# Kernel tuning notes

Measured on AMD Instinct MI355X. Metric: run time of the kernel, lower is better.

The kernel has to match this reference:

```python
import jax, jax.numpy as jnp
import numpy as np

B, T, H = 64, 2048, 64  # basins, daily timesteps, MLP hidden width


def _mlp(x, W1, b1, W2, b2, W3, b3, W4, b4):
    # x: [..., 4] -> [..., 5]; tanh hidden layers, linear head
    h = jnp.tanh(x @ W1 + b1)
    h = jnp.tanh(h @ W2 + b2)
    h = jnp.tanh(h @ W3 + b3)
    return h @ W4 + b4


def _step(x):
    # smooth step function from the torch module
    return (jnp.tanh(5.0 * x) + 1.0) * 0.5


def _interp(series, t):
    # linear interpolation of per-basin forcing series [B, T] at scalar time t
    # (time grid is the integer daily grid 0..T-1, matching time_series)
    n = series.shape[1]
    i0 = jnp.clip(jnp.floor(t).astype(jnp.int32), 0, n - 2)
    frac = t - i0.astype(series.dtype)
    pair = jax.lax.dynamic_slice_in_dim(series, i0, 2, axis=1)  # [B, 2]
    return pair[:, 0] * (1.0 - frac) + pair[:, 1] * frac


def _forward(s_snow, s_water, precp_series, tmean_series, lday_series, time_series,
             W1, b1, W2, b2, W3, b3, W4, b4):
    params = (W1, b1, W2, b2, W3, b3, W4, b4)

    def rhs(t, y):  # y: [B, 2]
        s0, s1 = y[:, 0], y[:, 1]
        precp = _interp(precp_series, t)
        temp = _interp(tmean_series, t)
        lday = _interp(lday_series, t)
        o = _mlp(jnp.stack([s0, s1, precp, temp], axis=-1), *params)  # [B, 5]
        # scale_target_vars=True branch
        p_snow = jax.nn.relu(jnp.sinh(o[:, 0]) * _step(-temp))
        p_rain = jax.nn.relu(jnp.sinh(o[:, 1]))
        m = jax.nn.relu(_step(s0) * jnp.sinh(o[:, 2]))
        et = _step(s1) * jnp.exp(o[:, 3]) * lday
        q = _step(s1) * jnp.exp(o[:, 4])
        return jnp.stack([p_snow - m, p_rain + m - et - q], axis=-1)

    y0 = jnp.stack([s_snow[:, 0], s_water[:, 0]], axis=-1)  # [B, 2]
    t0s = time_series[:-1]
    dts = time_series[1:] - time_series[:-1]

    def scan_step(y, td):  # classic RK4 between consecutive grid points
        t0, dt = td
        half = dt * 0.5
        k1 = rhs(t0, y)
        k2 = rhs(t0 + half, y + half * k1)
        k3 = rhs(t0 + half, y + half * k2)
        k4 = rhs(t0 + dt, y + dt * k3)
        y_next = y + (dt / 6.0) * (k1 + 2.0 * k2 + 2.0 * k3 + k4)
        return y_next, y_next

    _, ys = jax.lax.scan(scan_step, y0, (t0s, dts))  # [T-1, B, 2]
    y_full = jnp.concatenate([y0[None], ys], axis=0)  # [T, B, 2]
    y_full = jnp.transpose(y_full, (1, 0, 2))  # [B, T, 2]

    # final NN pass over the integrated states + raw forcing series
    inputs_nn = jnp.stack(
        [y_full[..., 0], y_full[..., 1], precp_series, tmean_series], axis=-1)  # [B, T, 4]
    q_out = _mlp(inputs_nn, *params)[..., -1]  # [B, T] (last output column = q)
    return q_out


def setup_inputs() -> dict:
    key = jax.random.key(0)
    ks = jax.random.split(key, 9)
    return {
        "s_snow": jax.random.uniform(ks[0], (B, T), dtype=jnp.float32),
        "s_water": jax.random.uniform(ks[1], (B, T), dtype=jnp.float32),
        "precp_series": jax.random.uniform(ks[2], (B, T), dtype=jnp.float32),
        "tmean_series": jax.random.normal(ks[3], (B, T), dtype=jnp.float32),
        "lday_series": jax.random.uniform(ks[4], (B, T), dtype=jnp.float32) * 0.5,
        "time_series": jnp.arange(T, dtype=jnp.float32),
        "W1": jax.random.normal(ks[5], (4, H), dtype=jnp.float32) / jnp.sqrt(4.0),
        "b1": jnp.zeros((H,), jnp.float32),
        "W2": jax.random.normal(ks[6], (H, H), dtype=jnp.float32) / jnp.sqrt(float(H)),
        "b2": jnp.zeros((H,), jnp.float32),
        "W3": jax.random.normal(ks[7], (H, H), dtype=jnp.float32) / jnp.sqrt(float(H)),
        "b3": jnp.zeros((H,), jnp.float32),
        "W4": jax.random.normal(ks[8], (H, 5), dtype=jnp.float32) * (0.1 / jnp.sqrt(float(H))),
        "b4": jnp.zeros((5,), jnp.float32),
    }


def reference(s_snow, s_water, precp_series, tmean_series, lday_series, time_series,
              W1, b1, W2, b2, W3, b3, W4, b4):
    return _forward(s_snow, s_water, precp_series, tmean_series, lday_series,
                    time_series, W1, b1, W2, b2, W3, b3, W4, b4)
```

## Files before the change

kernel.cpp:

```cpp
#include <hip/hip_runtime.h>
#include <cmath>

#define LOG2E 1.44269504088896340736f
#define TMAX 2048

#if __has_builtin(__builtin_amdgcn_exp2f)
#define EXP2F(x) __builtin_amdgcn_exp2f(x)
#else
#define EXP2F(x) exp2f(x)
#endif
#if __has_builtin(__builtin_amdgcn_rcpf)
#define RCPF(x) __builtin_amdgcn_rcpf(x)
#else
#define RCPF(x) (1.0f / (x))
#endif

typedef float float2v __attribute__((ext_vector_type(2)));
typedef float float4v __attribute__((ext_vector_type(4)));

__device__ __forceinline__ float fexp(float x)  { return EXP2F(x * LOG2E); }
__device__ __forceinline__ float ftanh(float x) { return 1.0f - 2.0f * RCPF(1.0f + EXP2F(x * (2.0f * LOG2E))); }
__device__ __forceinline__ float fstep(float x) { return RCPF(1.0f + EXP2F(x * (-10.0f * LOG2E))); }
__device__ __forceinline__ float fsinh(float x) { float e = fexp(x); return 0.5f * (e - RCPF(e)); }

__device__ __forceinline__ int fadd_i(int a, int b) {
    return __builtin_bit_cast(int, __builtin_bit_cast(float, a) + __builtin_bit_cast(float, b));
}

__device__ __forceinline__ float wave_sum63(float x) {
    int v = __builtin_bit_cast(int, x);
    v = fadd_i(v, __builtin_amdgcn_update_dpp(0, v, 0x111, 0xF, 0xF, true));
    v = fadd_i(v, __builtin_amdgcn_update_dpp(0, v, 0x112, 0xF, 0xF, true));
    v = fadd_i(v, __builtin_amdgcn_update_dpp(0, v, 0x114, 0xF, 0xF, true));
    v = fadd_i(v, __builtin_amdgcn_update_dpp(0, v, 0x118, 0xF, 0xF, true));
    v = fadd_i(v, __builtin_amdgcn_update_dpp(0, v, 0x142, 0xA, 0xF, true));
    v = fadd_i(v, __builtin_amdgcn_update_dpp(0, v, 0x143, 0xC, 0xF, true));
    return __builtin_bit_cast(float, v);
}

__device__ __forceinline__ float rl(float x, int l) {
    return __builtin_bit_cast(float, __builtin_amdgcn_readlane(__builtin_bit_cast(int, x), l));
}

__device__ __forceinline__ float2v pk_fma(float2v a, float2v b, float2v c) {
    float2v d;
    asm("v_pk_fma_f32 %0, %1, %2, %3" : "=v"(d) : "v"(a), "v"(b), "v"(c));
    return d;
}

__device__ __forceinline__ float2v vlo(float4v v) { return __builtin_shufflevector(v, v, 0, 1); }
__device__ __forceinline__ float2v vhi(float4v v) { return __builtin_shufflevector(v, v, 2, 3); }

__global__ __launch_bounds__(256, 1)
void exphydro_kernel(const float* __restrict__ g_snow, const float* __restrict__ g_water,
                     const float* __restrict__ g_pr, const float* __restrict__ g_tm,
                     const float* __restrict__ g_ld, const float* __restrict__ g_t,
                     const float* __restrict__ W1, const float* __restrict__ b1,
                     const float* __restrict__ W2, const float* __restrict__ b2,
                     const float* __restrict__ W3, const float* __restrict__ b3,
                     const float* __restrict__ W4, const float* __restrict__ b4,
                     float* __restrict__ out, int T)
{
    const int tid  = threadIdx.x;
    const int lane = tid & 63;
    const int wid  = tid >> 6;
    const int b    = blockIdx.x;

    __shared__ __align__(16) float4v s_f[TMAX];
    __shared__ __align__(16) float hcopy[4][64];
    __shared__ __align__(16) float partA[4][64];
    __shared__ __align__(16) float partB[4][64];

    for (int i = tid; i < T; i += 256) {
        s_f[i] = float4v{g_pr[b * T + i], g_tm[b * T + i], g_ld[b * T + i], g_t[i]};
    }

    float w1r[4];
#pragma unroll
    for (int j = 0; j < 4; ++j) w1r[j] = W1[j * 64 + lane];
    float b1v = b1[lane];

    float2v w2s[8], w3s[8];
#pragma unroll
    for (int k = 0; k < 8; ++k) {
        int r = 16 * wid + 2 * k;
        w2s[k] = float2v{W2[r * 64 + lane], W2[(r + 1) * 64 + lane]};
        w3s[k] = float2v{W3[r * 64 + lane], W3[(r + 1) * 64 + lane]};
    }
    float b2v = (wid == 0) ? b2[lane] : 0.0f;
    float b3v = (wid == 0) ? b3[lane] : 0.0f;
    float w4r[5], b4r[5];
#pragma unroll
    for (int k = 0; k < 5; ++k) { w4r[k] = W4[lane * 5 + k]; b4r[k] = b4[k]; }

    __syncthreads();

    auto quarter_dot = [&](const float* hq, const float2v (&w)[8], float bias) -> float {
        float4v q0 = *reinterpret_cast<const float4v*>(hq + 0);
        float4v q1 = *reinterpret_cast<const float4v*>(hq + 4);
        float4v q2 = *reinterpret_cast<const float4v*>(hq + 8);
        float4v q3 = *reinterpret_cast<const float4v*>(hq + 12);
        float2v a0 = float2v{bias, 0.0f}, a1 = float2v{0.0f, 0.0f};
        a0 = pk_fma(w[0], vlo(q0), a0); a1 = pk_fma(w[1], vhi(q0), a1);
        a0 = pk_fma(w[2], vlo(q1), a0); a1 = pk_fma(w[3], vhi(q1), a1);
        a0 = pk_fma(w[4], vlo(q2), a0); a1 = pk_fma(w[5], vhi(q2), a1);
        a0 = pk_fma(w[6], vlo(q3), a0); a1 = pk_fma(w[7], vhi(q3), a1);
        float2v s = a0 + a1;
        return s.x + s.y;
    };

    auto mlp_o63 = [&](float h1, float* o) {
        float* hown = &hcopy[wid][0];
        const float* hq = hown + 16 * wid;
        hown[lane] = h1;
        partA[wid][lane] = quarter_dot(hq, w2s, b2v);
        __syncthreads();
        float h2 = ftanh((partA[0][lane] + partA[1][lane]) + (partA[2][lane] + partA[3][lane]));
        hown[lane] = h2;
        partB[wid][lane] = quarter_dot(hq, w3s, b3v);
        __syncthreads();
        float h3 = ftanh((partB[0][lane] + partB[1][lane]) + (partB[2][lane] + partB[3][lane]));
#pragma unroll
        for (int k = 0; k < 5; ++k) o[k] = wave_sum63(w4r[k] * h3) + b4r[k];
    };

    auto rhs = [&](float base, float y0v, float y1v, float ld, float snt,
                   float& d0, float& d1, float& o4) {
        float h1 = ftanh(fmaf(w1r[0], y0v, fmaf(w1r[1], y1v, base)));
        float o[5];
        mlp_o63(h1, o);
        float psnow = fmaxf(0.0f, fsinh(o[0]) * snt);
        float prain = fmaxf(0.0f, fsinh(o[1]));
        float melt  = fmaxf(0.0f, fstep(y0v) * fsinh(o[2]));
        float eq    = fstep(y1v) * fmaf(fexp(o[3]), ld, fexp(o[4]));
        float d0l = psnow - melt;
        float d1l = (prain + melt) - eq;
        d0 = rl(d0l, 63);
        d1 = rl(d1l, 63);
        o4 = o[4];
    };

    float y0v = g_snow[b * T];
    float y1v = g_water[b * T];

    for (int st = 0; st < T - 1; ++st) {
        float4v fc = s_f[st];
        float4v fn = s_f[st + 1];

        float dt = fn.w - fc.w, half = 0.5f * dt, c6 = dt * (1.0f / 6.0f);
        float prH = 0.5f * (fc.x + fn.x);
        float tmH = 0.5f * (fc.y + fn.y);
        float ldH = 0.5f * (fc.z + fn.z);
        float snA = fstep(-fc.y), snH = fstep(-tmH), snC = fstep(-fn.y);
        float baseA = fmaf(w1r[2], fc.x, fmaf(w1r[3], fc.y, b1v));
        float baseH = fmaf(w1r[2], prH,  fmaf(w1r[3], tmH,  b1v));
        float baseC = fmaf(w1r[2], fn.x, fmaf(w1r[3], fn.y, b1v));

        float k1a, k1b, k2a, k2b, k3a, k3b, k4a, k4b, o4a, o4x;
        rhs(baseA, y0v, y1v, fc.z, snA, k1a, k1b, o4a);
        if (tid == 63) out[b * T + st] = o4a;
        rhs(baseH, fmaf(half, k1a, y0v), fmaf(half, k1b, y1v), ldH, snH, k2a, k2b, o4x);
        rhs(baseH, fmaf(half, k2a, y0v), fmaf(half, k2b, y1v), ldH, snH, k3a, k3b, o4x);
        rhs(baseC, fmaf(dt, k3a, y0v),   fmaf(dt, k3b, y1v),   fn.z, snC, k4a, k4b, o4x);

        y0v = fmaf(c6, (k1a + k4a) + 2.0f * (k2a + k3a), y0v);
        y1v = fmaf(c6, (k1b + k4b) + 2.0f * (k2b + k3b), y1v);
    }

    {
        float4v fL = s_f[T - 1];
        float base = fmaf(w1r[2], fL.x, fmaf(w1r[3], fL.y, b1v));
        float h1 = ftanh(fmaf(w1r[0], y0v, fmaf(w1r[1], y1v, base)));
        float o[5];
        mlp_o63(h1, o);
        if (tid == 63) out[b * T + (T - 1)] = o[4];
    }
}

extern "C" void kernel_launch(void* const* d_in, const int* in_sizes, int n_in,
                              void* d_out, int out_size, void* d_ws, size_t ws_size,
                              hipStream_t stream) {
    const float* g_snow  = (const float*)d_in[0];
    const float* g_water = (const float*)d_in[1];
    const float* g_pr    = (const float*)d_in[2];
    const float* g_tm    = (const float*)d_in[3];
    const float* g_ld    = (const float*)d_in[4];
    const float* g_t     = (const float*)d_in[5];
    const float* W1 = (const float*)d_in[6];
    const float* b1 = (const float*)d_in[7];
    const float* W2 = (const float*)d_in[8];
    const float* b2 = (const float*)d_in[9];
    const float* W3 = (const float*)d_in[10];
    const float* b3 = (const float*)d_in[11];
    const float* W4 = (const float*)d_in[12];
    const float* b4 = (const float*)d_in[13];

    const int T = in_sizes[5];
    const int B = in_sizes[0] / T;

    exphydro_kernel<<<dim3(B), dim3(256), 0, stream>>>(
        g_snow, g_water, g_pr, g_tm, g_ld, g_t,
        W1, b1, W2, b2, W3, b3, W4, b4,
        (float*)d_out, T);
}
```

Baseline: 5.845 ms.

## Compute layer-2 slice per wave with quad reductions, drop one barrier per MLP

Each wave now computes its own 16 columns of layer 2 redundantly from the full h1, with four lanes per output column and a DPP quad sum. The result goes to wave-private shared memory, so the block barrier between layers 2 and 3 is removed. Layer 3 keeps its cross-wave split, and the partial buffers now alternate between two sets across RK stages so one barrier per MLP call remains safe. The cost is extra quad-reduction instructions and wave-local shared-memory traffic, and correctness relies on wave-synchronous visibility of the LDS writes to hs.

```diff
diff --git a/kernel.cpp b/kernel.cpp
--- a/kernel.cpp
+++ b/kernel.cpp
@@ -35,6 +35,13 @@
     v = fadd_i(v, __builtin_amdgcn_update_dpp(0, v, 0x118, 0xF, 0xF, true));
     v = fadd_i(v, __builtin_amdgcn_update_dpp(0, v, 0x142, 0xA, 0xF, true));
     v = fadd_i(v, __builtin_amdgcn_update_dpp(0, v, 0x143, 0xC, 0xF, true));
+    return __builtin_bit_cast(float, v);
+}
+
+__device__ __forceinline__ float quad_sum(float x) {
+    int v = __builtin_bit_cast(int, x);
+    v = fadd_i(v, __builtin_amdgcn_update_dpp(0, v, 0xB1, 0xF, 0xF, true));
+    v = fadd_i(v, __builtin_amdgcn_update_dpp(0, v, 0x4E, 0xF, 0xF, true));
     return __builtin_bit_cast(float, v);
 }
 
@@ -65,11 +72,14 @@
     const int lane = tid & 63;
     const int wid  = tid >> 6;
     const int b    = blockIdx.x;
+    const int qk   = lane & 3;
+    const int qo   = lane >> 2;
+    const int col2 = 16 * wid + qo;
 
     __shared__ __align__(16) float4v s_f[TMAX];
-    __shared__ __align__(16) float hcopy[4][64];
-    __shared__ __align__(16) float partA[4][64];
-    __shared__ __align__(16) float partB[4][64];
+    __shared__ __align__(16) float hc[4][64];
+    __shared__ __align__(16) float hs[4][16];
+    __shared__ __align__(16) float partAB[2][4][64];
 
     for (int i = tid; i < T; i += 256) {
         s_f[i] = float4v{g_pr[b * T + i], g_tm[b * T + i], g_ld[b * T + i], g_t[i]};
@@ -79,15 +89,19 @@
 #pragma unroll
     for (int j = 0; j < 4; ++j) w1r[j] = W1[j * 64 + lane];
     float b1v = b1[lane];
-
-    float2v w2s[8], w3s[8];
+    float2v w2n[8];
+#pragma unroll
+    for (int k = 0; k < 8; ++k) {
+        int r = qk * 16 + 2 * k;
+        w2n[k] = float2v{W2[r * 64 + col2], W2[(r + 1) * 64 + col2]};
+    }
+    float b2s = b2[col2];
+    float2v w3s[8];
 #pragma unroll
     for (int k = 0; k < 8; ++k) {
         int r = 16 * wid + 2 * k;
-        w2s[k] = float2v{W2[r * 64 + lane], W2[(r + 1) * 64 + lane]};
         w3s[k] = float2v{W3[r * 64 + lane], W3[(r + 1) * 64 + lane]};
     }
-    float b2v = (wid == 0) ? b2[lane] : 0.0f;
     float b3v = (wid == 0) ? b3[lane] : 0.0f;
     float w4r[5], b4r[5];
 #pragma unroll
@@ -95,40 +109,44 @@
 
     __syncthreads();
 
-    auto quarter_dot = [&](const float* hq, const float2v (&w)[8], float bias) -> float {
+    auto mlp_o63 = [&](float h1, float (*part)[64], float* o) {
+        hc[wid][lane] = h1;
+        const float* hq = &hc[wid][qk * 16];
         float4v q0 = *reinterpret_cast<const float4v*>(hq + 0);
         float4v q1 = *reinterpret_cast<const float4v*>(hq + 4);
         float4v q2 = *reinterpret_cast<const float4v*>(hq + 8);
         float4v q3 = *reinterpret_cast<const float4v*>(hq + 12);
-        float2v a0 = float2v{bias, 0.0f}, a1 = float2v{0.0f, 0.0f};
-        a0 = pk_fma(w[0], vlo(q0), a0); a1 = pk_fma(w[1], vhi(q0), a1);
-        a0 = pk_fma(w[2], vlo(q1), a0); a1 = pk_fma(w[3], vhi(q1), a1);
-        a0 = pk_fma(w[4], vlo(q2), a0); a1 = pk_fma(w[5], vhi(q2), a1);
-        a0 = pk_fma(w[6], vlo(q3), a0); a1 = pk_fma(w[7], vhi(q3), a1);
-        float2v s = a0 + a1;
-        return s.x + s.y;
-    };
-
-    auto mlp_o63 = [&](float h1, float* o) {
-        float* hown = &hcopy[wid][0];
-        const float* hq = hown + 16 * wid;
-        hown[lane] = h1;
-        partA[wid][lane] = quarter_dot(hq, w2s, b2v);
+        float2v a0 = float2v{0.0f, 0.0f}, a1 = float2v{0.0f, 0.0f};
+        a0 = pk_fma(w2n[0], vlo(q0), a0); a1 = pk_fma(w2n[1], vhi(q0), a1);
+        a0 = pk_fma(w2n[2], vlo(q1), a0); a1 = pk_fma(w2n[3], vhi(q1), a1);
+        a0 = pk_fma(w2n[4], vlo(q2), a0); a1 = pk_fma(w2n[5], vhi(q2), a1);
+        a0 = pk_fma(w2n[6], vlo(q3), a0); a1 = pk_fma(w2n[7], vhi(q3), a1);
+        float2v sa = a0 + a1;
+        float t2 = quad_sum(sa.x + sa.y);
+        float h2 = ftanh(t2 + b2s);
+        if (qk == 0) hs[wid][qo] = h2;
+        float4v r0 = *reinterpret_cast<const float4v*>(&hs[wid][0]);
+        float4v r1 = *reinterpret_cast<const float4v*>(&hs[wid][4]);
+        float4v r2 = *reinterpret_cast<const float4v*>(&hs[wid][8]);
+        float4v r3 = *reinterpret_cast<const float4v*>(&hs[wid][12]);
+        float2v c0 = float2v{b3v, 0.0f}, c1 = float2v{0.0f, 0.0f};
+        c0 = pk_fma(w3s[0], vlo(r0), c0); c1 = pk_fma(w3s[1], vhi(r0), c1);
+        c0 = pk_fma(w3s[2], vlo(r1), c0); c1 = pk_fma(w3s[3], vhi(r1), c1);
+        c0 = pk_fma(w3s[4], vlo(r2), c0); c1 = pk_fma(w3s[5], vhi(r2), c1);
+        c0 = pk_fma(w3s[6], vlo(r3), c0); c1 = pk_fma(w3s[7], vhi(r3), c1);
+        float2v sc = c0 + c1;
+        part[wid][lane] = sc.x + sc.y;
         __syncthreads();
-        float h2 = ftanh((partA[0][lane] + partA[1][lane]) + (partA[2][lane] + partA[3][lane]));
-        hown[lane] = h2;
-        partB[wid][lane] = quarter_dot(hq, w3s, b3v);
-        __syncthreads();
-        float h3 = ftanh((partB[0][lane] + partB[1][lane]) + (partB[2][lane] + partB[3][lane]));
+        float h3 = ftanh((part[0][lane] + part[1][lane]) + (part[2][lane] + part[3][lane]));
 #pragma unroll
         for (int k = 0; k < 5; ++k) o[k] = wave_sum63(w4r[k] * h3) + b4r[k];
     };
 
     auto rhs = [&](float base, float y0v, float y1v, float ld, float snt,
-                   float& d0, float& d1, float& o4) {
+                   float (*part)[64], float& d0, float& d1, float& o4) {
         float h1 = ftanh(fmaf(w1r[0], y0v, fmaf(w1r[1], y1v, base)));
         float o[5];
-        mlp_o63(h1, o);
+        mlp_o63(h1, part, o);
         float psnow = fmaxf(0.0f, fsinh(o[0]) * snt);
         float prain = fmaxf(0.0f, fsinh(o[1]));
         float melt  = fmaxf(0.0f, fstep(y0v) * fsinh(o[2]));
@@ -157,11 +175,11 @@
         float baseC = fmaf(w1r[2], fn.x, fmaf(w1r[3], fn.y, b1v));
 
         float k1a, k1b, k2a, k2b, k3a, k3b, k4a, k4b, o4a, o4x;
-        rhs(baseA, y0v, y1v, fc.z, snA, k1a, k1b, o4a);
+        rhs(baseA, y0v, y1v, fc.z, snA, partAB[0], k1a, k1b, o4a);
         if (tid == 63) out[b * T + st] = o4a;
-        rhs(baseH, fmaf(half, k1a, y0v), fmaf(half, k1b, y1v), ldH, snH, k2a, k2b, o4x);
-        rhs(baseH, fmaf(half, k2a, y0v), fmaf(half, k2b, y1v), ldH, snH, k3a, k3b, o4x);
-        rhs(baseC, fmaf(dt, k3a, y0v),   fmaf(dt, k3b, y1v),   fn.z, snC, k4a, k4b, o4x);
+        rhs(baseH, fmaf(half, k1a, y0v), fmaf(half, k1b, y1v), ldH, snH, partAB[1], k2a, k2b, o4x);
+        rhs(baseH, fmaf(half, k2a, y0v), fmaf(half, k2b, y1v), ldH, snH, partAB[0], k3a, k3b, o4x);
+        rhs(baseC, fmaf(dt, k3a, y0v),   fmaf(dt, k3b, y1v),   fn.z, snC, partAB[1], k4a, k4b, o4x);
 
         y0v = fmaf(c6, (k1a + k4a) + 2.0f * (k2a + k3a), y0v);
         y1v = fmaf(c6, (k1b + k4b) + 2.0f * (k2b + k3b), y1v);
@@ -172,7 +190,7 @@
         float base = fmaf(w1r[2], fL.x, fmaf(w1r[3], fL.y, b1v));
         float h1 = ftanh(fmaf(w1r[0], y0v, fmaf(w1r[1], y1v, base)));
         float o[5];
-        mlp_o63(h1, o);
+        mlp_o63(h1, partAB[0], o);
         if (tid == 63) out[b * T + (T - 1)] = o[4];
     }
 }
```

Result: faster. 5.143 ms (-12.0%).
